# Performance work log

Measured on AMD Instinct MI355X. Metric: run time of the kernel, lower is better.

Reference implementation:

```python
import jax, jax.numpy as jnp
import numpy as np

S, B, C, H, E, V, T = 196, 64, 1024, 1024, 512, 32000, 20


def setup_inputs() -> dict:
    key = jax.random.key(0)
    ks = jax.random.split(key, 16)

    def w(k, shape, fan_in):
        return (jax.random.normal(k, shape, jnp.float32) / np.sqrt(fan_in)).astype(jnp.float32)

    emb_W = w(ks[2], (V, E), E).at[0].set(0.0)  # padding_idx=0
    return {
        'ctx': jax.random.normal(ks[0], (S, B, C), jnp.float32),
        'y': jax.random.randint(ks[1], (T, B), 0, V, jnp.int32),
        'emb_W': emb_W,
        'att_ctx2ctx': w(ks[3], (C, C), C),
        'att_hid2ctx': w(ks[4], (H, C), H),
        'att_mlp': w(ks[5], (C,), C),
        'gru_W_ih': w(ks[6], (3 * H, E + C), E + C),
        'gru_b_ih': jnp.zeros((3 * H,), jnp.float32),
        'gru_W_hh': w(ks[7], (3 * H, H), H),
        'gru_b_hh': jnp.zeros((3 * H,), jnp.float32),
        'hid2out_W': w(ks[8], (E, H), H),
        'hid2out_b': jnp.zeros((E,), jnp.float32),
        'out_ctx_W': w(ks[9], (E, C), C),
        'out_ctx_b': jnp.zeros((E,), jnp.float32),
        'out2prob_W': w(ks[10], (V, E), E),
        'out2prob_b': jnp.zeros((V,), jnp.float32),
    }


def reference(ctx, y, emb_W, att_ctx2ctx, att_hid2ctx, att_mlp,
              gru_W_ih, gru_b_ih, gru_W_hh, gru_b_hh,
              hid2out_W, hid2out_b, out_ctx_W, out_ctx_b,
              out2prob_W, out2prob_b):
    hidden = gru_W_hh.shape[1]
    y_emb = emb_W[y]                                        # [T, B, E]
    ctx_proj = jnp.einsum('sbc,cm->sbm', ctx, att_ctx2ctx)  # precompute ctx2ctx(ctx)

    def gru_cell(x, h):
        gi = x @ gru_W_ih.T + gru_b_ih
        gh = h @ gru_W_hh.T + gru_b_hh
        i_r, i_z, i_n = jnp.split(gi, 3, axis=-1)
        h_r, h_z, h_n = jnp.split(gh, 3, axis=-1)
        r = jax.nn.sigmoid(i_r + h_r)
        z = jax.nn.sigmoid(i_z + h_z)
        n = jnp.tanh(i_n + r * h_n)
        return (1.0 - z) * n + z * h

    def step(h, inp):
        y_t, tgt = inp                                      # [B,E], [B]
        # MLP attention over source positions S
        scores = jnp.einsum('sbm,m->sb', jnp.tanh(ctx_proj + (h @ att_hid2ctx)[None]), att_mlp)
        alpha = jax.nn.softmax(scores, axis=0)              # [S, B]
        z_t = jnp.einsum('sb,sbc->bc', alpha, ctx)          # [B, C]
        ht = gru_cell(jnp.concatenate([y_t, z_t], axis=-1), h)
        logit = jnp.tanh(ht @ hid2out_W.T + hid2out_b)      # hid2out (tanh FF)
        logit = logit + y_t                                 # prev2out
        logit = logit + z_t @ out_ctx_W.T + out_ctx_b       # ctx2out
        log_p = jax.nn.log_softmax(jnp.tanh(logit) @ out2prob_W.T + out2prob_b, axis=-1)
        mask = (tgt != 0).astype(log_p.dtype)               # NLLLoss ignore_index=0, sum
        nll = -jnp.sum(jnp.take_along_axis(log_p, tgt[:, None], axis=1)[:, 0] * mask)
        return ht, nll

    h0 = jnp.zeros((y.shape[1], hidden), ctx.dtype)         # dec_init='zero'
    _, nlls = jax.lax.scan(step, h0, (y_emb[:-1], y[1:]))
    return jnp.sum(nlls)
```

## Files before the change

kernel.cpp:

```cpp
#include <hip/hip_runtime.h>
#include <math.h>

#define TS_ 19

typedef float f32x4 __attribute__((ext_vector_type(4)));
typedef short s16x8 __attribute__((ext_vector_type(8)));
typedef unsigned short us;
typedef unsigned char uc;

__device__ __forceinline__ float sigmoidf_(float x) { return 1.f / (1.f + __expf(-x)); }

__device__ __forceinline__ float fast_tanh(float x) {
    float ax = fabsf(x);
    float e = __expf(-2.f * ax);
    float r = (1.f - e) * __builtin_amdgcn_rcpf(1.f + e);
    return copysignf(r, x);
}

__device__ __forceinline__ us f2b(float x) {
    union { float f; unsigned u; } v; v.f = x;
    unsigned r = v.u + 0x7fffu + ((v.u >> 16) & 1u);
    return (us)(r >> 16);
}
__device__ __forceinline__ float b2f(us u) {
    union { unsigned u; float f; } v; v.u = ((unsigned)u) << 16; return v.f;
}
__device__ __forceinline__ uc f2e4m3(float x) {
    return (uc)(__builtin_amdgcn_cvt_pk_fp8_f32(x, 0.f, 0, false) & 0xff);
}

#define MFMA(a, b, c) __builtin_amdgcn_mfma_f32_16x16x32_bf16((a), (b), (c), 0, 0, 0)
#define MFMA8(a, b, c) __builtin_amdgcn_mfma_f32_16x16x32_fp8_fp8((a), (b), (c), 0, 0, 0)

__device__ __forceinline__ f32x4 zero4() { return (f32x4){0.f, 0.f, 0.f, 0.f}; }

__device__ __forceinline__ f32x4 wg16(const us* ap, const us* bp, int nk, f32x4 acc) {
#pragma unroll 4
    for (int k = 0; k < nk; k += 32)
        acc = MFMA(*(const s16x8*)(ap + k), *(const s16x8*)(bp + k), acc);
    return acc;
}

__device__ __forceinline__ void gload_lds16(const void* g, void* l) {
    __builtin_amdgcn_global_load_lds(
        (const __attribute__((address_space(1))) unsigned int*)g,
        (__attribute__((address_space(3))) unsigned int*)l, 16, 0, 0);
}

__global__ __launch_bounds__(256) void k_cvt(const float* __restrict__ in,
                                             us* __restrict__ out, long n) {
    long i = ((long)blockIdx.x * 256 + threadIdx.x) * 4;
    long stride = (long)gridDim.x * 1024;
    for (; i < n; i += stride) {
        float4 v = *(const float4*)(in + i);
        ushort4 o = { f2b(v.x), f2b(v.y), f2b(v.z), f2b(v.w) };
        *(ushort4*)(out + i) = o;
    }
}

__global__ __launch_bounds__(256) void k_cvt8(const float* __restrict__ in,
                                              uc* __restrict__ out, long n) {
    long i = ((long)blockIdx.x * 256 + threadIdx.x) * 8;
    long stride = (long)gridDim.x * 2048;
    for (; i < n; i += stride) {
        float4 v0 = *(const float4*)(in + i);
        float4 v1 = *(const float4*)(in + i + 4);
        int lo = __builtin_amdgcn_cvt_pk_fp8_f32(v0.x, v0.y, 0, false);
        lo = __builtin_amdgcn_cvt_pk_fp8_f32(v0.z, v0.w, lo, true);
        int hi = __builtin_amdgcn_cvt_pk_fp8_f32(v1.x, v1.y, 0, false);
        hi = __builtin_amdgcn_cvt_pk_fp8_f32(v1.z, v1.w, hi, true);
        int2 o = { lo, hi };
        *(int2*)(out + i) = o;
    }
}

__global__ void k_tcvt(const float* __restrict__ in, us* __restrict__ out) {
    __shared__ float tile[32][33];
    int bx = blockIdx.x * 32, by = blockIdx.y * 32;
    int x = threadIdx.x, y0 = threadIdx.y;
    for (int yy = y0; yy < 32; yy += 8) tile[yy][x] = in[(by + yy) * 1024 + bx + x];
    __syncthreads();
    for (int yy = y0; yy < 32; yy += 8) out[(bx + yy) * 1024 + by + x] = f2b(tile[x][yy]);
}

__global__ __launch_bounds__(256) void k_yemb(const int* __restrict__ y,
                                              const float* __restrict__ embW,
                                              us* __restrict__ xc) {
    int t = blockIdx.x >> 6, b = blockIdx.x & 63;
    int row = y[t * 64 + b];
    const float* src = embW + (long)row * 512;
    us* dst = xc + (long)(t * 64 + b) * 2560;
    for (int e = threadIdx.x; e < 512; e += 256) dst[e] = f2b(src[e]);
}

__global__ __launch_bounds__(256) void k_prepw(const float* __restrict__ Wih,
                                               const float* __restrict__ Whh,
                                               us* __restrict__ Wg) {
    int n = blockIdx.x, tid = threadIdx.x;
    int cl = n >> 10;
    if (cl < 2) {
        long base = (long)n * 2560;
        const float* wi = Wih + (long)n * 1536;
        const float* wh = Whh + (long)n * 1024;
        for (int k = tid; k < 1536; k += 256) Wg[base + k] = f2b(wi[k]);
        for (int k = tid; k < 1024; k += 256) Wg[base + 1536 + k] = f2b(wh[k]);
    } else if (cl == 2) {
        long base = 5242880L + (long)(n - 2048) * 1536;
        const float* wi = Wih + (long)n * 1536;
        for (int k = tid; k < 1536; k += 256) Wg[base + k] = f2b(wi[k]);
    } else {
        long base = 6815744L + (long)(n - 3072) * 1024;
        const float* wh = Whh + (long)(n - 1024) * 1024;
        for (int k = tid; k < 1024; k += 256) Wg[base + k] = f2b(wh[k]);
    }
}

__global__ __launch_bounds__(256) void k_gemm(const us* __restrict__ A,
                                              const us* __restrict__ Bt,
                                              us* __restrict__ Cb) {
    __shared__ us As[8192], Bs[8192];
    int tid = threadIdx.x, lane = tid & 63, w = tid >> 6;
    int mr = lane & 15, kb = lane >> 4;
    int bm = blockIdx.x % 98, bn = blockIdx.x / 98;
    long m0 = (long)bm * 128;
    int n0 = bn * 128;
    int wr = w >> 1, wc = w & 1;
    int srow = w * 32 + (lane >> 3);
    int ib = (lane & 7) * 16;

    f32x4 acc[4][4];
#pragma unroll
    for (int i = 0; i < 4; i++)
#pragma unroll
        for (int j = 0; j < 4; j++) acc[i][j] = zero4();

    for (int kt = 0; kt < 16; ++kt) {
        int k0 = kt * 64;
        __syncthreads();
#pragma unroll
        for (int c = 0; c < 4; ++c) {
            int r = srow + c * 8;
            int sw = (ib ^ ((r & 7) << 4)) >> 1;
            gload_lds16(A + (m0 + r) * 1024 + k0 + sw, &As[w * 2048 + c * 512]);
            gload_lds16(Bt + (long)(n0 + r) * 1024 + k0 + sw, &Bs[w * 2048 + c * 512]);
        }
        __syncthreads();
#pragma unroll
        for (int ks = 0; ks < 2; ++ks) {
            s16x8 af[4], bf[4];
#pragma unroll
            for (int mt = 0; mt < 4; ++mt) {
                int r = wr * 64 + mt * 16 + mr;
                af[mt] = *(const s16x8*)&As[(r * 128 + ((ks * 64 + kb * 16) ^ ((r & 7) << 4))) >> 1];
            }
#pragma unroll
            for (int nt = 0; nt < 4; ++nt) {
                int r = wc * 64 + nt * 16 + mr;
                bf[nt] = *(const s16x8*)&Bs[(r * 128 + ((ks * 64 + kb * 16) ^ ((r & 7) << 4))) >> 1];
            }
#pragma unroll
            for (int mt = 0; mt < 4; ++mt)
#pragma unroll
                for (int nt = 0; nt < 4; ++nt)
                    acc[mt][nt] = MFMA(af[mt], bf[nt], acc[mt][nt]);
        }
    }
#pragma unroll
    for (int mt = 0; mt < 4; ++mt)
#pragma unroll
        for (int nt = 0; nt < 4; ++nt)
#pragma unroll
            for (int j = 0; j < 4; ++j)
                Cb[(m0 + wr * 64 + mt * 16 + kb * 4 + j) * 1024 +
                   n0 + wc * 64 + nt * 16 + mr] = f2b(acc[mt][nt][j]);
}

__global__ __launch_bounds__(256) void k_hproj(const us* __restrict__ hcur,
                                               const us* __restrict__ attbf,
                                               float* __restrict__ hpp) {
    int tid = threadIdx.x, lane = tid & 63, w = tid >> 6;
    int vn0 = (blockIdx.x >> 1) * 16, kc = blockIdx.x & 1;
    int m0 = w * 16, mr = lane & 15, kb = lane >> 4;
    const us* ap = hcur + (long)(m0 + mr) * 1024 + kc * 512 + kb * 8;
    const us* bp = attbf + (long)(vn0 + mr) * 1024 + kc * 512 + kb * 8;
    f32x4 acc = wg16(ap, bp, 512, zero4());
#pragma unroll
    for (int j = 0; j < 4; ++j)
        hpp[(long)kc * 65536 + (long)(m0 + kb * 4 + j) * 1024 + vn0 + mr] = acc[j];
}

__global__ __launch_bounds__(1024) void k_scores(const us* __restrict__ cpb,
                                                 const float* __restrict__ hpp,
                                                 const float* __restrict__ mlp,
                                                 float* __restrict__ scores) {
    __shared__ float hp[1024];
    __shared__ float ml[1024];
    int tid = threadIdx.x;
    int b = blockIdx.x >> 2, sq = blockIdx.x & 3;
    hp[tid] = hpp[(long)b * 1024 + tid] + hpp[65536 + (long)b * 1024 + tid];
    ml[tid] = mlp[tid];
    __syncthreads();
    int wv = tid >> 6, lane = tid & 63;
    int s0 = sq * 49;
    for (int s = s0 + wv; s < s0 + 49; s += 16) {
        const us* cp = cpb + (long)(s * 64 + b) * 1024 + lane * 16;
        s16x8 c0 = *(const s16x8*)cp;
        s16x8 c1 = *(const s16x8*)(cp + 8);
        int e0 = lane * 16;
        float acc = 0.f;
#pragma unroll
        for (int j = 0; j < 8; ++j)
            acc += fast_tanh(b2f((us)c0[j]) + hp[e0 + j]) * ml[e0 + j];
#pragma unroll
        for (int j = 0; j < 8; ++j)
            acc += fast_tanh(b2f((us)c1[j]) + hp[e0 + 8 + j]) * ml[e0 + 8 + j];
#pragma unroll
        for (int off = 32; off; off >>= 1) acc += __shfl_xor(acc, off, 64);
        if (lane == 0) scores[b * 196 + s] = acc;
    }
}

__global__ __launch_bounds__(512) void k_z(const float* __restrict__ scores,
                                           const us* __restrict__ ctxbf,
                                           us* __restrict__ xc, int t) {
    __shared__ float red[512];
    __shared__ float als[196];
    __shared__ float zp[256];
    int tid = threadIdx.x, b = blockIdx.x >> 2, ch = blockIdx.x & 3;
    const float* sc = scores + b * 196;
    float lm = (tid < 196) ? sc[tid] : -1e30f;
    red[tid] = lm; __syncthreads();
    for (int st = 256; st; st >>= 1) { if (tid < st) red[tid] = fmaxf(red[tid], red[tid + st]); __syncthreads(); }
    float m = red[0]; __syncthreads();
    float ls = (tid < 196) ? __expf(sc[tid] - m) : 0.f;
    red[tid] = ls; __syncthreads();
    for (int st = 256; st; st >>= 1) { if (tid < st) red[tid] += red[tid + st]; __syncthreads(); }
    float inv = 1.f / red[0];
    if (tid < 196) als[tid] = ls * inv;
    __syncthreads();
    int c = ch * 256 + (tid & 255);
    int sh = tid >> 8;
    const us* cp = ctxbf + (long)b * 1024 + c;
    float a0 = 0.f;
    int sb = sh * 98;
    for (int s = sb; s < sb + 98; s += 2) {
        a0 += als[s] * b2f(cp[(long)s * 65536]) +
              als[s + 1] * b2f(cp[(long)(s + 1) * 65536]);
    }
    if (sh) zp[tid & 255] = a0;
    __syncthreads();
    if (!sh) {
        a0 += zp[tid & 255];
        xc[(long)(t * 64 + b) * 2560 + 512 + c] = f2b(a0);
    }
}

__global__ __launch_bounds__(512) void k_gruh2(us* __restrict__ xc,
                                               const us* __restrict__ Wg,
                                               const float* __restrict__ bih,
                                               const float* __restrict__ bhh,
                                               float* __restrict__ hf32,
                                               us* __restrict__ ht_all, int t) {
    __shared__ float lg[2048];
    int tid = threadIdx.x, lane = tid & 63, w = tid >> 6;
    int mr = lane & 15, kb = lane >> 4;
    int g = w >> 1, kh = w & 1;
    int mq = blockIdx.x & 3, jt = blockIdx.x >> 2;
    int m0 = mq * 16, j0 = jt * 16;
    const us* xr = xc + (long)t * 163840 + (long)(m0 + mr) * 2560;

    f32x4 acc = zero4();
    if (g == 0) {
        acc = wg16(xr + kh * 1280 + kb * 8,
                   Wg + (long)(j0 + mr) * 2560 + kh * 1280 + kb * 8, 1280, acc);
    } else if (g == 1) {
        acc = wg16(xr + kh * 1280 + kb * 8,
                   Wg + (long)(1024 + j0 + mr) * 2560 + kh * 1280 + kb * 8, 1280, acc);
    } else if (g == 2) {
        acc = wg16(xr + kh * 768 + kb * 8,
                   Wg + 5242880L + (long)(j0 + mr) * 1536 + kh * 768 + kb * 8, 768, acc);
    } else {
        acc = wg16(xr + 1536 + kh * 512 + kb * 8,
                   Wg + 6815744L + (long)(j0 + mr) * 1024 + kh * 512 + kb * 8, 512, acc);
    }
#pragma unroll
    for (int j = 0; j < 4; ++j)
        lg[(g * 2 + kh) * 256 + (kb * 4 + j) * 16 + mr] = acc[j];
    __syncthreads();

    if (tid < 256) {
        int ml = tid >> 4, jj = tid & 15;
        int b = m0 + ml, j = j0 + jj;
        float gr = lg[0 * 256 + ml * 16 + jj] + lg[1 * 256 + ml * 16 + jj];
        float gz = lg[2 * 256 + ml * 16 + jj] + lg[3 * 256 + ml * 16 + jj];
        float gi = lg[4 * 256 + ml * 16 + jj] + lg[5 * 256 + ml * 16 + jj];
        float gh = lg[6 * 256 + ml * 16 + jj] + lg[7 * 256 + ml * 16 + jj];
        float r  = sigmoidf_(gr + bih[j] + bhh[j]);
        float zz = sigmoidf_(gz + bih[1024 + j] + bhh[1024 + j]);
        float n  = fast_tanh(gi + bih[2048 + j] + r * (gh + bhh[2048 + j]));
        float h = (1.f - zz) * n + zz * hf32[b * 1024 + j];
        hf32[b * 1024 + j] = h;
        us hb = f2b(h);
        ht_all[(long)((t + 1) * 64 + b) * 1024 + j] = hb;
        if (t < TS_ - 1) xc[(long)((t + 1) * 64 + b) * 2560 + 1536 + j] = hb;
    }
}

__global__ __launch_bounds__(256) void k_outb(const us* __restrict__ ht_all,
                                              const us* __restrict__ xc,
                                              const us* __restrict__ h2obf,
                                              const float* __restrict__ h2ob,
                                              const us* __restrict__ octxbf,
                                              const float* __restrict__ octxb,
                                              us* __restrict__ obf_all,
                                              uc* __restrict__ obf8) {
    int tid = threadIdx.x, lane = tid & 63, w = tid >> 6;
    int mr = lane & 15, kb = lane >> 4;
    int m0 = blockIdx.x * 64;
    int n0 = blockIdx.y * 256 + w * 64;
    f32x4 a1[4][4], a2[4][4];
#pragma unroll
    for (int i = 0; i < 4; i++)
#pragma unroll
        for (int j = 0; j < 4; j++) { a1[i][j] = zero4(); a2[i][j] = zero4(); }

    for (int k0 = 0; k0 < 1024; k0 += 32) {
        s16x8 bf[4], af[4];
#pragma unroll
        for (int nt = 0; nt < 4; ++nt)
            bf[nt] = *(const s16x8*)(h2obf + (long)(n0 + nt * 16 + mr) * 1024 + k0 + kb * 8);
#pragma unroll
        for (int mt = 0; mt < 4; ++mt)
            af[mt] = *(const s16x8*)(ht_all + (long)(64 + m0 + mt * 16 + mr) * 1024 + k0 + kb * 8);
#pragma unroll
        for (int mt = 0; mt < 4; ++mt)
#pragma unroll
            for (int nt = 0; nt < 4; ++nt)
                a1[mt][nt] = MFMA(af[mt], bf[nt], a1[mt][nt]);
    }
    for (int k0 = 0; k0 < 1024; k0 += 32) {
        s16x8 bf[4], af[4];
#pragma unroll
        for (int nt = 0; nt < 4; ++nt)
            bf[nt] = *(const s16x8*)(octxbf + (long)(n0 + nt * 16 + mr) * 1024 + k0 + kb * 8);
#pragma unroll
        for (int mt = 0; mt < 4; ++mt)
            af[mt] = *(const s16x8*)(xc + (long)(m0 + mt * 16 + mr) * 2560 + 512 + k0 + kb * 8);
#pragma unroll
        for (int mt = 0; mt < 4; ++mt)
#pragma unroll
            for (int nt = 0; nt < 4; ++nt)
                a2[mt][nt] = MFMA(af[mt], bf[nt], a2[mt][nt]);
    }
#pragma unroll
    for (int mt = 0; mt < 4; ++mt)
#pragma unroll
        for (int nt = 0; nt < 4; ++nt) {
            int e = n0 + nt * 16 + mr;
            float b1 = h2ob[e], b2 = octxb[e];
#pragma unroll
            for (int j = 0; j < 4; ++j) {
                long row = m0 + mt * 16 + kb * 4 + j;
                float ye = b2f(xc[row * 2560 + e]);
                float val = fast_tanh(fast_tanh(a1[mt][nt][j] + b1) + ye + a2[mt][nt][j] + b2);
                obf_all[(row << 9) + e] = f2b(val);
                obf8[(row << 9) + e] = f2e4m3(val);
            }
        }
}

__global__ __launch_bounds__(256) void k_vocab8(const uc* __restrict__ obf8,
                                                const uc* __restrict__ o2p8,
                                                const float* __restrict__ o2pb,
                                                float* __restrict__ pm,
                                                float* __restrict__ ps) {
    __shared__ uc As[8192], Bs[8192];
    int tid = threadIdx.x, lane = tid & 63, w = tid >> 6;
    int mr = lane & 15, kb = lane >> 4;
    int xq = blockIdx.x & 7, idx = blockIdx.x >> 3;
    int nb = xq * 32 + idx / 10, mb = idx % 10;
    int m0 = mb * 128, n0 = nb * 128;
    int wr = w >> 1, wc = w & 1;
    int srow = w * 32 + (lane >> 2);
    int ib = (lane & 3) * 16;

    f32x4 acc[4][4];
#pragma unroll
    for (int i = 0; i < 4; i++)
#pragma unroll
        for (int j = 0; j < 4; j++) acc[i][j] = zero4();

    for (int kt = 0; kt < 8; ++kt) {
        int k0 = kt * 64;
        __syncthreads();
#pragma unroll
        for (int c = 0; c < 2; ++c) {
            int r = srow + c * 16;
            int sw = ib ^ ((r & 6) << 3);
            gload_lds16(obf8 + (long)(m0 + r) * 512 + k0 + sw, &As[w * 2048 + c * 1024]);
            gload_lds16(o2p8 + (long)(n0 + r) * 512 + k0 + sw, &Bs[w * 2048 + c * 1024]);
        }
        __syncthreads();
#pragma unroll
        for (int ks = 0; ks < 2; ++ks) {
            long af[4], bf[4];
#pragma unroll
            for (int mt = 0; mt < 4; ++mt) {
                int r = wr * 64 + mt * 16 + mr;
                af[mt] = *(const long*)&As[r * 64 + ((ks * 32 + kb * 8) ^ ((r & 6) << 3))];
            }
#pragma unroll
            for (int nt = 0; nt < 4; ++nt) {
                int r = wc * 64 + nt * 16 + mr;
                bf[nt] = *(const long*)&Bs[r * 64 + ((ks * 32 + kb * 8) ^ ((r & 6) << 3))];
            }
#pragma unroll
            for (int mt = 0; mt < 4; ++mt)
#pragma unroll
                for (int nt = 0; nt < 4; ++nt)
                    acc[mt][nt] = MFMA8(af[mt], bf[nt], acc[mt][nt]);
        }
    }

    int n0w = n0 + wc * 64;
    float bv[4];
#pragma unroll
    for (int nt = 0; nt < 4; ++nt) {
        int vn = n0w + nt * 16 + mr;
        bv[nt] = (vn < 32000) ? o2pb[vn] : -1e30f;
    }
#pragma unroll
    for (int mt = 0; mt < 4; ++mt)
#pragma unroll
        for (int j = 0; j < 4; ++j) {
            float x0 = acc[mt][0][j] + bv[0];
            float x1 = acc[mt][1][j] + bv[1];
            float x2 = acc[mt][2][j] + bv[2];
            float x3 = acc[mt][3][j] + bv[3];
            float m = fmaxf(fmaxf(x0, x1), fmaxf(x2, x3));
            float s = __expf(x0 - m) + __expf(x1 - m) + __expf(x2 - m) + __expf(x3 - m);
#pragma unroll
            for (int off = 1; off <= 8; off <<= 1) {
                float mo = __shfl_xor(m, off, 64), so = __shfl_xor(s, off, 64);
                float nm = fmaxf(m, mo);
                s = s * __expf(m - nm) + so * __expf(mo - nm);
                m = nm;
            }
            if (mr == 0) {
                int row = m0 + wr * 64 + mt * 16 + kb * 4 + j;
                pm[(long)(nb * 2 + wc) * 1280 + row] = m;
                ps[(long)(nb * 2 + wc) * 1280 + row] = s;
            }
        }
}

__global__ __launch_bounds__(64) void k_lseb(const float* __restrict__ pm,
                                             const float* __restrict__ ps,
                                             const us* __restrict__ obf_all,
                                             const float* __restrict__ o2pW,
                                             const float* __restrict__ o2pb,
                                             const int* __restrict__ y,
                                             float* __restrict__ out) {
    int r = blockIdx.x, lane = threadIdx.x;
    int t = r >> 6, b = r & 63;
    int tgt = y[(t + 1) * 64 + b];
    float m = -1e30f, s = 0.f;
    for (int p = lane; p < 512; p += 64) {
        float mi = pm[(long)p * 1280 + r], si = ps[(long)p * 1280 + r];
        float nm = fmaxf(m, mi);
        s = s * __expf(m - nm) + si * __expf(mi - nm);
        m = nm;
    }
#pragma unroll
    for (int off = 32; off; off >>= 1) {
        float mo = __shfl_xor(m, off, 64), so = __shfl_xor(s, off, 64);
        float nm = fmaxf(m, mo);
        s = s * __expf(m - nm) + so * __expf(mo - nm);
        m = nm;
    }
    float d = 0.f;
    const float* wr = o2pW + (long)tgt * 512;
#pragma unroll
    for (int k = 0; k < 8; ++k)
        d += b2f(obf_all[(long)r * 512 + lane + k * 64]) * wr[lane + k * 64];
#pragma unroll
    for (int off = 32; off; off >>= 1) d += __shfl_xor(d, off, 64);
    if (lane == 0 && tgt != 0)
        atomicAdd(out, (m + __logf(s)) - (d + o2pb[tgt]));
}

extern "C" void kernel_launch(void* const* d_in, const int* in_sizes, int n_in,
                              void* d_out, int out_size, void* d_ws, size_t ws_size,
                              hipStream_t stream) {
    const float* ctx     = (const float*)d_in[0];
    const int*   y       = (const int*)d_in[1];
    const float* embW    = (const float*)d_in[2];
    const float* att_c2c = (const float*)d_in[3];
    const float* att_h2c = (const float*)d_in[4];
    const float* mlp     = (const float*)d_in[5];
    const float* Wih     = (const float*)d_in[6];
    const float* bih     = (const float*)d_in[7];
    const float* Whh     = (const float*)d_in[8];
    const float* bhh     = (const float*)d_in[9];
    const float* h2oW    = (const float*)d_in[10];
    const float* h2ob    = (const float*)d_in[11];
    const float* octxW   = (const float*)d_in[12];
    const float* octxb   = (const float*)d_in[13];
    const float* o2pW    = (const float*)d_in[14];
    const float* o2pb    = (const float*)d_in[15];
    float* out = (float*)d_out;

    char* base = (char*)d_ws;
    us* ctxbf   = (us*)base; base += 25690112L;
    us* cpbf    = (us*)base; base += 25690112L;
    us* c2cT    = (us*)base; base += 2097152L;
    us* attbf   = (us*)base; base += 2097152L;
    us* Wg      = (us*)base; base += 15728640L;
    us* h2obf   = (us*)base; base += 1048576L;
    us* octxbf  = (us*)base; base += 1048576L;
    uc* o2p8    = (uc*)base; base += 16777216L;
    us* xc      = (us*)base; base += 6225920L;
    us* ht_all  = (us*)base; base += 2621440L;
    us* obf_all = (us*)base; base += 1310720L;
    uc* obf8    = (uc*)base; base += 655360L;
    float* hf32   = (float*)base; base += 262144L;
    float* hpp    = (float*)base; base += 524288L;
    float* scb    = (float*)base; base += 50176L;
    float* pm   = (float*)cpbf;
    float* ps   = pm + 655360L;

    (void)hipMemsetAsync(d_out, 0, sizeof(float), stream);
    (void)hipMemsetAsync(hf32, 0, 262144, stream);
    (void)hipMemsetAsync(ht_all, 0, 131072, stream);
    (void)hipMemsetAsync(obf_all + 1216L * 512, 0, 65536, stream);
    (void)hipMemsetAsync(obf8 + 1216L * 512, 0, 32768, stream);
    (void)hipMemsetAsync(o2p8 + 16384000L, 0, 393216, stream);
    (void)hipMemsetAsync(xc, 0, 6225920, stream);

    k_yemb<<<TS_ * 64, 256, 0, stream>>>(y, embW, xc);
    k_tcvt<<<dim3(32, 32), dim3(32, 8), 0, stream>>>(att_c2c, c2cT);
    k_tcvt<<<dim3(32, 32), dim3(32, 8), 0, stream>>>(att_h2c, attbf);
    k_cvt<<<2048, 256, 0, stream>>>(ctx, ctxbf, 12845056L);
    k_cvt<<<512, 256, 0, stream>>>(h2oW, h2obf, 524288L);
    k_cvt<<<512, 256, 0, stream>>>(octxW, octxbf, 524288L);
    k_cvt8<<<2048, 256, 0, stream>>>(o2pW, o2p8, 16384000L);
    k_prepw<<<4096, 256, 0, stream>>>(Wih, Whh, Wg);
    k_gemm<<<784, 256, 0, stream>>>(ctxbf, c2cT, cpbf);

    for (int t = 0; t < TS_; t++) {
        k_hproj<<<128, 256, 0, stream>>>(ht_all + (long)t * 65536, attbf, hpp);
        k_scores<<<256, 1024, 0, stream>>>(cpbf, hpp, mlp, scb);
        k_z<<<256, 512, 0, stream>>>(scb, ctxbf, xc, t);
        k_gruh2<<<256, 512, 0, stream>>>(xc, Wg, bih, bhh, hf32, ht_all, t);
    }

    k_outb<<<dim3(19, 2), 256, 0, stream>>>(ht_all, xc, h2obf, h2ob, octxbf, octxb,
                                            obf_all, obf8);
    k_vocab8<<<2560, 256, 0, stream>>>(obf8, o2p8, o2pb, pm, ps);
    k_lseb<<<1216, 64, 0, stream>>>(pm, ps, obf_all, o2pW, o2pb, y, out);
}
```

Baseline: 975.4 us.

## Retile GRU step to cover full batch per block and widen outb grid

```diff
diff --git a/kernel.cpp b/kernel.cpp
--- a/kernel.cpp
+++ b/kernel.cpp
@@ -243,6 +243,7 @@
     const us* cp = ctxbf + (long)b * 1024 + c;
     float a0 = 0.f;
     int sb = sh * 98;
+#pragma unroll 4
     for (int s = sb; s < sb + 98; s += 2) {
         a0 += als[s] * b2f(cp[(long)s * 65536]) +
               als[s + 1] * b2f(cp[(long)(s + 1) * 65536]);
@@ -255,46 +256,65 @@
     }
 }
 
-__global__ __launch_bounds__(512) void k_gruh2(us* __restrict__ xc,
+__global__ __launch_bounds__(512) void k_gruh3(us* __restrict__ xc,
                                                const us* __restrict__ Wg,
                                                const float* __restrict__ bih,
                                                const float* __restrict__ bhh,
                                                float* __restrict__ hf32,
                                                us* __restrict__ ht_all, int t) {
-    __shared__ float lg[2048];
+    __shared__ float lg[8192];
     int tid = threadIdx.x, lane = tid & 63, w = tid >> 6;
     int mr = lane & 15, kb = lane >> 4;
     int g = w >> 1, kh = w & 1;
-    int mq = blockIdx.x & 3, jt = blockIdx.x >> 2;
-    int m0 = mq * 16, j0 = jt * 16;
-    const us* xr = xc + (long)t * 163840 + (long)(m0 + mr) * 2560;
-
-    f32x4 acc = zero4();
-    if (g == 0) {
-        acc = wg16(xr + kh * 1280 + kb * 8,
-                   Wg + (long)(j0 + mr) * 2560 + kh * 1280 + kb * 8, 1280, acc);
-    } else if (g == 1) {
-        acc = wg16(xr + kh * 1280 + kb * 8,
-                   Wg + (long)(1024 + j0 + mr) * 2560 + kh * 1280 + kb * 8, 1280, acc);
+    int j0 = blockIdx.x * 16;
+    const us* xbase = xc + (long)t * 163840 + (long)mr * 2560 + kb * 8;
+
+    const us* ap;
+    const us* bp;
+    int Kh;
+    if (g < 2) {
+        Kh = 1280;
+        ap = xbase + kh * 1280;
+        bp = Wg + (long)(g * 1024 + j0 + mr) * 2560 + kh * 1280 + kb * 8;
     } else if (g == 2) {
-        acc = wg16(xr + kh * 768 + kb * 8,
-                   Wg + 5242880L + (long)(j0 + mr) * 1536 + kh * 768 + kb * 8, 768, acc);
+        Kh = 768;
+        ap = xbase + kh * 768;
+        bp = Wg + 5242880L + (long)(j0 + mr) * 1536 + kh * 768 + kb * 8;
     } else {
-        acc = wg16(xr + 1536 + kh * 512 + kb * 8,
-                   Wg + 6815744L + (long)(j0 + mr) * 1024 + kh * 512 + kb * 8, 512, acc);
-    }
-#pragma unroll
-    for (int j = 0; j < 4; ++j)
-        lg[(g * 2 + kh) * 256 + (kb * 4 + j) * 16 + mr] = acc[j];
+        Kh = 512;
+        ap = xbase + 1536 + kh * 512;
+        bp = Wg + 6815744L + (long)(j0 + mr) * 1024 + kh * 512 + kb * 8;
+    }
+
+    f32x4 acc[4];
+#pragma unroll
+    for (int i = 0; i < 4; i++) acc[i] = zero4();
+
+#pragma unroll 2
+    for (int k = 0; k < Kh; k += 32) {
+        s16x8 bfrag = *(const s16x8*)(bp + k);
+#pragma unroll
+        for (int mt = 0; mt < 4; ++mt) {
+            s16x8 afrag = *(const s16x8*)(ap + mt * 40960 + k);
+            acc[mt] = MFMA(afrag, bfrag, acc[mt]);
+        }
+    }
+#pragma unroll
+    for (int mt = 0; mt < 4; ++mt)
+#pragma unroll
+        for (int j = 0; j < 4; ++j)
+            lg[(g * 2 + kh) * 1024 + (mt * 16 + kb * 4 + j) * 16 + mr] = acc[mt][j];
     __syncthreads();
 
-    if (tid < 256) {
-        int ml = tid >> 4, jj = tid & 15;
-        int b = m0 + ml, j = j0 + jj;
-        float gr = lg[0 * 256 + ml * 16 + jj] + lg[1 * 256 + ml * 16 + jj];
-        float gz = lg[2 * 256 + ml * 16 + jj] + lg[3 * 256 + ml * 16 + jj];
-        float gi = lg[4 * 256 + ml * 16 + jj] + lg[5 * 256 + ml * 16 + jj];
-        float gh = lg[6 * 256 + ml * 16 + jj] + lg[7 * 256 + ml * 16 + jj];
+#pragma unroll
+    for (int q = 0; q < 2; ++q) {
+        int idx = tid + q * 512;
+        int b = idx >> 4, jj = idx & 15;
+        int j = j0 + jj;
+        float gr = lg[0 * 1024 + b * 16 + jj] + lg[1 * 1024 + b * 16 + jj];
+        float gz = lg[2 * 1024 + b * 16 + jj] + lg[3 * 1024 + b * 16 + jj];
+        float gi = lg[4 * 1024 + b * 16 + jj] + lg[5 * 1024 + b * 16 + jj];
+        float gh = lg[6 * 1024 + b * 16 + jj] + lg[7 * 1024 + b * 16 + jj];
         float r  = sigmoidf_(gr + bih[j] + bhh[j]);
         float zz = sigmoidf_(gz + bih[1024 + j] + bhh[1024 + j]);
         float n  = fast_tanh(gi + bih[2048 + j] + r * (gh + bhh[2048 + j]));
@@ -317,55 +337,37 @@
     int tid = threadIdx.x, lane = tid & 63, w = tid >> 6;
     int mr = lane & 15, kb = lane >> 4;
     int m0 = blockIdx.x * 64;
-    int n0 = blockIdx.y * 256 + w * 64;
-    f32x4 a1[4][4], a2[4][4];
-#pragma unroll
-    for (int i = 0; i < 4; i++)
-#pragma unroll
-        for (int j = 0; j < 4; j++) { a1[i][j] = zero4(); a2[i][j] = zero4(); }
-
+    int n0 = blockIdx.y * 64;
+    int e = n0 + w * 16 + mr;
+    const us* bb1 = h2obf + (long)e * 1024 + kb * 8;
+    const us* bb2 = octxbf + (long)e * 1024 + kb * 8;
+    const us* ab1 = ht_all + (long)(64 + m0 + mr) * 1024 + kb * 8;
+    const us* ab2 = xc + (long)(m0 + mr) * 2560 + 512 + kb * 8;
+
+    f32x4 a1[4], a2[4];
+#pragma unroll
+    for (int i = 0; i < 4; i++) { a1[i] = zero4(); a2[i] = zero4(); }
+
+#pragma unroll 2
     for (int k0 = 0; k0 < 1024; k0 += 32) {
-        s16x8 bf[4], af[4];
-#pragma unroll
-        for (int nt = 0; nt < 4; ++nt)
-            bf[nt] = *(const s16x8*)(h2obf + (long)(n0 + nt * 16 + mr) * 1024 + k0 + kb * 8);
-#pragma unroll
-        for (int mt = 0; mt < 4; ++mt)
-            af[mt] = *(const s16x8*)(ht_all + (long)(64 + m0 + mt * 16 + mr) * 1024 + k0 + kb * 8);
-#pragma unroll
-        for (int mt = 0; mt < 4; ++mt)
-#pragma unroll
-            for (int nt = 0; nt < 4; ++nt)
-                a1[mt][nt] = MFMA(af[mt], bf[nt], a1[mt][nt]);
-    }
-    for (int k0 = 0; k0 < 1024; k0 += 32) {
-        s16x8 bf[4], af[4];
-#pragma unroll
-        for (int nt = 0; nt < 4; ++nt)
-            bf[nt] = *(const s16x8*)(octxbf + (long)(n0 + nt * 16 + mr) * 1024 + k0 + kb * 8);
-#pragma unroll
-        for (int mt = 0; mt < 4; ++mt)
-            af[mt] = *(const s16x8*)(xc + (long)(m0 + mt * 16 + mr) * 2560 + 512 + k0 + kb * 8);
-#pragma unroll
-        for (int mt = 0; mt < 4; ++mt)
-#pragma unroll
-            for (int nt = 0; nt < 4; ++nt)
-                a2[mt][nt] = MFMA(af[mt], bf[nt], a2[mt][nt]);
-    }
+        s16x8 b1 = *(const s16x8*)(bb1 + k0);
+        s16x8 b2 = *(const s16x8*)(bb2 + k0);
+#pragma unroll
+        for (int mt = 0; mt < 4; ++mt) {
+            a1[mt] = MFMA(*(const s16x8*)(ab1 + mt * 16384 + k0), b1, a1[mt]);
+            a2[mt] = MFMA(*(const s16x8*)(ab2 + mt * 40960 + k0), b2, a2[mt]);
+        }
+    }
+    float b1v = h2ob[e], b2v = octxb[e];
 #pragma unroll
     for (int mt = 0; mt < 4; ++mt)
 #pragma unroll
-        for (int nt = 0; nt < 4; ++nt) {
-            int e = n0 + nt * 16 + mr;
-            float b1 = h2ob[e], b2 = octxb[e];
-#pragma unroll
-            for (int j = 0; j < 4; ++j) {
-                long row = m0 + mt * 16 + kb * 4 + j;
-                float ye = b2f(xc[row * 2560 + e]);
-                float val = fast_tanh(fast_tanh(a1[mt][nt][j] + b1) + ye + a2[mt][nt][j] + b2);
-                obf_all[(row << 9) + e] = f2b(val);
-                obf8[(row << 9) + e] = f2e4m3(val);
-            }
+        for (int j = 0; j < 4; ++j) {
+            long row = m0 + mt * 16 + kb * 4 + j;
+            float ye = b2f(xc[row * 2560 + e]);
+            float val = fast_tanh(fast_tanh(a1[mt][j] + b1v) + ye + a2[mt][j] + b2v);
+            obf_all[(row << 9) + e] = f2b(val);
+            obf8[(row << 9) + e] = f2e4m3(val);
         }
 }
 
@@ -551,10 +553,10 @@
         k_hproj<<<128, 256, 0, stream>>>(ht_all + (long)t * 65536, attbf, hpp);
         k_scores<<<256, 1024, 0, stream>>>(cpbf, hpp, mlp, scb);
         k_z<<<256, 512, 0, stream>>>(scb, ctxbf, xc, t);
-        k_gruh2<<<256, 512, 0, stream>>>(xc, Wg, bih, bhh, hf32, ht_all, t);
-    }
-
-    k_outb<<<dim3(19, 2), 256, 0, stream>>>(ht_all, xc, h2obf, h2ob, octxbf, octxb,
+        k_gruh3<<<64, 512, 0, stream>>>(xc, Wg, bih, bhh, hf32, ht_all, t);
+    }
+
+    k_outb<<<dim3(19, 8), 256, 0, stream>>>(ht_all, xc, h2obf, h2ob, octxbf, octxb,
                                             obf_all, obf8);
     k_vocab8<<<2560, 256, 0, stream>>>(obf8, o2p8, o2pb, pm, ps);
     k_lseb<<<1216, 64, 0, stream>>>(pm, ps, obf_all, o2pW, o2pb, y, out);
```

Result: slower. 1.406 ms (+44.1%).
